# Performance work log

Measured on AMD Instinct MI355X. Metric: run time of the kernel, lower is better.

## Reference

```python
import jax, jax.numpy as jnp
import numpy as np

KSIZE = 11
SIGMA = 1.5
CHANNELS = 1


def _gaussian_kernel(size=KSIZE, sigma=SIGMA, channels=CHANNELS):
    coords = jnp.arange(size, dtype=jnp.float32) - size // 2
    g = jnp.exp(-coords ** 2 / (2.0 * sigma ** 2))
    g = g / g.sum()
    k2d = jnp.outer(g, g)  # [k, k]
    # depthwise kernel, OIHW with I=1 per group
    return jnp.broadcast_to(k2d, (channels, 1, size, size))


def _dwconv(x, k):
    pad = KSIZE // 2
    return jax.lax.conv_general_dilated(
        x, k, window_strides=(1, 1), padding=[(pad, pad), (pad, pad)],
        dimension_numbers=('NCHW', 'OIHW', 'NCHW'),
        feature_group_count=CHANNELS)


def setup_inputs() -> dict:
    key = jax.random.key(0)
    k1, k2 = jax.random.split(key)
    x_hat = jax.random.normal(k1, (64, 1, 512, 512), dtype=jnp.float32)
    x = jax.random.normal(k2, (64, 1, 512, 512), dtype=jnp.float32)
    kernel = _gaussian_kernel()
    return {"x_hat": x_hat, "x": x, "kernel": kernel}


def reference(x_hat, x, kernel):
    C1, C2 = 0.01 ** 2, 0.03 ** 2
    # shift [-1,1] -> [0,1]
    a = (x + 1.0) / 2.0          # 'x' in _ssim
    b = (x_hat + 1.0) / 2.0      # 'y' in _ssim
    mu_x = _dwconv(a, kernel)
    mu_y = _dwconv(b, kernel)
    mu_x2 = mu_x ** 2
    mu_y2 = mu_y ** 2
    mu_xy = mu_x * mu_y
    sig_x = _dwconv(a * a, kernel) - mu_x2
    sig_y = _dwconv(b * b, kernel) - mu_y2
    sig_xy = _dwconv(a * b, kernel) - mu_xy
    num = (2.0 * mu_xy + C1) * (2.0 * sig_xy + C2)
    den = (mu_x2 + mu_y2 + C1) * (sig_x + sig_y + C2)
    ssim = (num / (den + 1e-08)).mean()
    return 1.0 - ssim
```

## Files before the change

kernel.cpp:

```cpp
#include <hip/hip_runtime.h>
#include <stdint.h>

#define IMG_W 512
#define IMG_H 512
#define RH    64
#define KS    11
#define KR    5
#define OFF   8
#define LROW  (OFF + IMG_W + OFF)
#define CH    KS
#define NROWS (RH + 2*KR)
#define NCH   7

__global__ __launch_bounds__(512, 4)
void ssim_main(const float* __restrict__ xhat,
               const float* __restrict__ x,
               const float* __restrict__ kern,
               float* __restrict__ accum)
{
    __shared__ float rowA[CH][LROW];
    __shared__ float rowB[CH][LROW];
    __shared__ float red[8];

    const int tid   = threadIdx.x;
    const int lane  = tid & 63;
    const int wid   = tid >> 6;
    const int c     = tid;
    const int img   = blockIdx.x >> 3;
    const int strip = blockIdx.x & 7;
    const int R0    = strip * RH;
    const float* xp = x    + (size_t)img * (IMG_W * IMG_H);
    const float* hp = xhat + (size_t)img * (IMG_W * IMG_H);

    float g[KS];
    {
        const float inv = rsqrtf(kern[5 * KS + 5]);
        #pragma unroll
        for (int i = 0; i < KS; ++i) g[i] = kern[5 * KS + i] * inv;
    }

    {
        float4* a4 = (float4*)&rowA[0][0];
        float4* b4 = (float4*)&rowB[0][0];
        #pragma unroll 1
        for (int i = tid; i < (CH * LROW) / 4; i += 512) {
            a4[i] = make_float4(0.f, 0.f, 0.f, 0.f);
            b4[i] = make_float4(0.f, 0.f, 0.f, 0.f);
        }
    }

    float hist[5][KS];
    float acc = 0.f;
    const float C1 = 1e-4f, C2 = 9e-4f;

    #pragma unroll 1
    for (int chk = 0; chk < NCH; ++chk) {
        __syncthreads();

        #pragma unroll
        for (int k = 0; k < 6; ++k) {
            const int q = wid + 8 * k;
            if (q < 4 * CH) {
                const int j  = q >> 2;
                const int rr = chk * CH + j;
                if (rr < NROWS) {
                    const int f  = (q >> 1) & 1;
                    const int h  = q & 1;
                    const int ri = R0 - KR + rr;
                    float* ldsbase = f ? &rowB[j][OFF + h * 256]
                                       : &rowA[j][OFF + h * 256];
                    if (ri >= 0 && ri < IMG_H) {
                        const float* gsrc = (f ? hp : xp)
                            + (size_t)ri * IMG_W + h * 256 + lane * 4;
                        __builtin_amdgcn_global_load_lds(
                            (const __attribute__((address_space(1))) void*)gsrc,
                            (__attribute__((address_space(3))) void*)ldsbase,
                            16, 0, 0);
                    } else {
                        *(float4*)(ldsbase + lane * 4) =
                            make_float4(0.f, 0.f, 0.f, 0.f);
                    }
                }
            }
        }
        __syncthreads();

        #pragma unroll
        for (int p = 0; p < CH; ++p) {
            const int rr = chk * CH + p;
            if (rr < NROWS) {
                const int ib = OFF + c - 6;
                float wa[12], wb[12];
                #pragma unroll
                for (int m = 0; m < 6; ++m) {
                    const float2 ta = *(const float2*)&rowA[p][ib + 2 * m];
                    const float2 tb = *(const float2*)&rowB[p][ib + 2 * m];
                    wa[2 * m] = ta.x; wa[2 * m + 1] = ta.y;
                    wb[2 * m] = tb.x; wb[2 * m + 1] = tb.y;
                }

                float h0 = 0.f, h1 = 0.f, h2 = 0.f, h3 = 0.f, h4 = 0.f;
                #pragma unroll
                for (int t = 0; t < KS; ++t) {
                    const float w  = g[t];
                    const float pa = wa[t + 1];
                    const float pb = wb[t + 1];
                    h0 = fmaf(w, pa,      h0);
                    h1 = fmaf(w, pb,      h1);
                    h2 = fmaf(w, pa * pa, h2);
                    h3 = fmaf(w, pb * pb, h3);
                    h4 = fmaf(w, pa * pb, h4);
                }
                hist[0][p] = h0; hist[1][p] = h1; hist[2][p] = h2;
                hist[3][p] = h3; hist[4][p] = h4;

                if (rr >= 2 * KR) {
                    float U = 0.f, V = 0.f, U2 = 0.f, V2 = 0.f, UVc = 0.f;
                    #pragma unroll
                    for (int t = 0; t < KS; ++t) {
                        const int slot = (p + 1 + t) % KS;
                        const float w = g[t];
                        U   = fmaf(w, hist[0][slot], U);
                        V   = fmaf(w, hist[1][slot], V);
                        U2  = fmaf(w, hist[2][slot], U2);
                        V2  = fmaf(w, hist[3][slot], V2);
                        UVc = fmaf(w, hist[4][slot], UVc);
                    }
                    const float pU = U + 1.f, pV = V + 1.f;
                    const float t1 = fmaf(0.5f,  pU * pV,            C1);
                    const float t2 = fmaf(0.5f,  fmaf(-U, V, UVc),   C2);
                    const float t3 = fmaf(0.25f, fmaf(pU, pU, pV*pV), C1);
                    const float e  = fmaf(-U, U, U2) + fmaf(-V, V, V2);
                    const float t4 = fmaf(0.25f, e,                  C2);
                    acc = fmaf(t1 * t2,
                               __builtin_amdgcn_rcpf(fmaf(t3, t4, 1e-8f)),
                               acc);
                }
            }
        }
    }

    #pragma unroll
    for (int o = 32; o > 0; o >>= 1) acc += __shfl_down(acc, o, 64);
    if (lane == 0) red[wid] = acc;
    __syncthreads();
    if (tid == 0) {
        float s = 0.f;
        #pragma unroll
        for (int w = 0; w < 8; ++w) s += red[w];
        atomicAdd(accum, s);
    }
}

__global__ void ssim_final(const float* __restrict__ accum,
                           float* __restrict__ out)
{
    out[0] = 1.0f - accum[0] * (1.0f / (64.0f * 512.0f * 512.0f));
}

extern "C" void kernel_launch(void* const* d_in, const int* in_sizes, int n_in,
                              void* d_out, int out_size, void* d_ws, size_t ws_size,
                              hipStream_t stream) {
    const float* xhat = (const float*)d_in[0];
    const float* xin  = (const float*)d_in[1];
    const float* kern = (const float*)d_in[2];
    float* out = (float*)d_out;
    float* ws  = (float*)d_ws;

    const int nimg   = in_sizes[0] / (IMG_W * IMG_H);
    const int strips = IMG_H / RH;
    const int nblk   = nimg * strips;

    hipMemsetAsync(ws, 0, sizeof(float), stream);
    ssim_main<<<nblk, 512, 0, stream>>>(xhat, xin, kern, ws);
    ssim_final<<<1, 1, 0, stream>>>(ws, out);
}
```

Baseline: 213.0 us.

## Merge squared-sum channels into one filtered sum and scalarize gaussian weights

```diff
diff --git a/kernel.cpp b/kernel.cpp
--- a/kernel.cpp
+++ b/kernel.cpp
@@ -12,7 +12,7 @@
 #define NROWS (RH + 2*KR)
 #define NCH   7
 
-__global__ __launch_bounds__(512, 4)
+__global__ __launch_bounds__(512, 3)
 void ssim_main(const float* __restrict__ xhat,
                const float* __restrict__ x,
                const float* __restrict__ kern,
@@ -36,7 +36,11 @@
     {
         const float inv = rsqrtf(kern[5 * KS + 5]);
         #pragma unroll
-        for (int i = 0; i < KS; ++i) g[i] = kern[5 * KS + i] * inv;
+        for (int i = 0; i < KS; ++i) {
+            const float v = kern[5 * KS + i] * inv;
+            g[i] = __builtin_bit_cast(float,
+                     __builtin_amdgcn_readfirstlane(__builtin_bit_cast(int, v)));
+        }
     }
 
     {
@@ -49,7 +53,7 @@
         }
     }
 
-    float hist[5][KS];
+    float hist[4][KS];
     float acc = 0.f;
     const float C1 = 1e-4f, C2 = 9e-4f;
 
@@ -99,39 +103,40 @@
                     wb[2 * m] = tb.x; wb[2 * m + 1] = tb.y;
                 }
 
-                float h0 = 0.f, h1 = 0.f, h2 = 0.f, h3 = 0.f, h4 = 0.f;
+                float hU = 0.f, hV = 0.f, hS = 0.f, hP = 0.f;
                 #pragma unroll
                 for (int t = 0; t < KS; ++t) {
                     const float w  = g[t];
                     const float pa = wa[t + 1];
                     const float pb = wb[t + 1];
-                    h0 = fmaf(w, pa,      h0);
-                    h1 = fmaf(w, pb,      h1);
-                    h2 = fmaf(w, pa * pa, h2);
-                    h3 = fmaf(w, pb * pb, h3);
-                    h4 = fmaf(w, pa * pb, h4);
+                    const float papa = pa * pa;
+                    const float sq   = fmaf(pb, pb, papa);
+                    const float pab  = pa * pb;
+                    hU = fmaf(w, pa,  hU);
+                    hV = fmaf(w, pb,  hV);
+                    hS = fmaf(w, sq,  hS);
+                    hP = fmaf(w, pab, hP);
                 }
-                hist[0][p] = h0; hist[1][p] = h1; hist[2][p] = h2;
-                hist[3][p] = h3; hist[4][p] = h4;
+                hist[0][p] = hU; hist[1][p] = hV;
+                hist[2][p] = hS; hist[3][p] = hP;
 
                 if (rr >= 2 * KR) {
-                    float U = 0.f, V = 0.f, U2 = 0.f, V2 = 0.f, UVc = 0.f;
+                    float U = 0.f, V = 0.f, S = 0.f, P = 0.f;
                     #pragma unroll
                     for (int t = 0; t < KS; ++t) {
                         const int slot = (p + 1 + t) % KS;
                         const float w = g[t];
-                        U   = fmaf(w, hist[0][slot], U);
-                        V   = fmaf(w, hist[1][slot], V);
-                        U2  = fmaf(w, hist[2][slot], U2);
-                        V2  = fmaf(w, hist[3][slot], V2);
-                        UVc = fmaf(w, hist[4][slot], UVc);
+                        U = fmaf(w, hist[0][slot], U);
+                        V = fmaf(w, hist[1][slot], V);
+                        S = fmaf(w, hist[2][slot], S);
+                        P = fmaf(w, hist[3][slot], P);
                     }
                     const float pU = U + 1.f, pV = V + 1.f;
-                    const float t1 = fmaf(0.5f,  pU * pV,            C1);
-                    const float t2 = fmaf(0.5f,  fmaf(-U, V, UVc),   C2);
-                    const float t3 = fmaf(0.25f, fmaf(pU, pU, pV*pV), C1);
-                    const float e  = fmaf(-U, U, U2) + fmaf(-V, V, V2);
-                    const float t4 = fmaf(0.25f, e,                  C2);
+                    const float t1 = fmaf(0.5f,  pU * pV,              C1);
+                    const float t2 = fmaf(0.5f,  fmaf(-U, V, P),       C2);
+                    const float t3 = fmaf(0.25f, fmaf(pU, pU, pV * pV), C1);
+                    const float e  = fmaf(-V, V, fmaf(-U, U, S));
+                    const float t4 = fmaf(0.25f, e,                    C2);
                     acc = fmaf(t1 * t2,
                                __builtin_amdgcn_rcpf(fmaf(t3, t4, 1e-8f)),
                                acc);
```

Measured after the change: 209.5 us. No clear change (-1.6%).
